# Optimization experiments

Hardware: AMD Instinct MI355X
Metric: run time of the kernel (lower is better)

Reference implementation:

```python
import jax, jax.numpy as jnp
import numpy as np

B, S, D, H = 4, 2048, 512, 8
DH = D // H  # 64


def setup_inputs() -> dict:
    key = jax.random.key(0)
    ks = jax.random.split(key, 7)
    scale = 1.0 / np.sqrt(D)
    return {
        "in_query": jax.random.normal(ks[0], (B, S, D), dtype=jnp.float32),
        "in_key": jax.random.normal(ks[1], (B, S, D), dtype=jnp.float32),
        "in_value": jax.random.normal(ks[2], (B, S, D), dtype=jnp.float32),
        "W_q": jax.random.normal(ks[3], (D, D), dtype=jnp.float32) * scale,
        "W_k": jax.random.normal(ks[4], (D, D), dtype=jnp.float32) * scale,
        "W_v": jax.random.normal(ks[5], (D, D), dtype=jnp.float32) * scale,
        "W_out": jax.random.normal(ks[6], (D, D), dtype=jnp.float32) * scale,
    }


def _split_heads(x):
    # [B, S, D] -> [B, H, S, DH]
    return x.reshape(B, S, H, DH).transpose(0, 2, 1, 3)


def reference(in_query, in_key, in_value, W_q, W_k, W_v, W_out):
    q = _split_heads(in_query @ W_q)   # [B,H,S,DH]
    k = _split_heads(in_key @ W_k)
    v = _split_heads(in_value @ W_v)
    scores = jnp.einsum("bhqd,bhkd->bhqk", q, k) / jnp.sqrt(jnp.float32(DH))
    attn = jax.nn.softmax(scores, axis=-1)  # dropout p=0 -> identity
    out = jnp.einsum("bhqk,bhkd->bhqd", attn, v)  # [B,H,S,DH]
    out = out.transpose(0, 2, 1, 3).reshape(B, S, D)
    return out @ W_out
```

## Files before the change

### kernel.cpp

```cpp
#include <hip/hip_runtime.h>
#include <hip/hip_bf16.h>
#include <cstdint>
#include <cstddef>


typedef __bf16 bf16;
typedef __attribute__((ext_vector_type(8))) __bf16 bf16x8;
typedef __attribute__((ext_vector_type(4))) __bf16 bf16x4;
typedef __attribute__((ext_vector_type(4))) float floatx4;

#define MFMA16(a, b, c) __builtin_amdgcn_mfma_f32_16x16x32_bf16(a, b, c, 0, 0, 0)

#define GLD16(gp, lp)                                              \
  __builtin_amdgcn_global_load_lds(                                \
      (const __attribute__((address_space(1))) unsigned int*)(gp), \
      (__attribute__((address_space(3))) unsigned int*)(lp), 16, 0, 0)

__device__ __forceinline__ void split2(float x, bf16& hi, bf16& lo) {
  hi = (bf16)x;
  lo = (bf16)(x - (float)hi);
}

__global__ __launch_bounds__(256) void k_split_w(
    const float* __restrict__ Wq, const float* __restrict__ Wk,
    const float* __restrict__ Wv, const float* __restrict__ Wo,
    bf16* __restrict__ wt_hi, bf16* __restrict__ wt_lo) {
  __shared__ float tile[64][65];
  const int w = blockIdx.z;
  const float* W = (w == 0) ? Wq : (w == 1) ? Wk : (w == 2) ? Wv : Wo;
  const int kb = blockIdx.y * 64, nb = blockIdx.x * 64;
  const int tid = threadIdx.x;
  const int col = tid & 63, rbase = tid >> 6;
#pragma unroll
  for (int i = 0; i < 16; i++) {
    int row = rbase + i * 4;
    tile[row][col] = W[(size_t)(kb + row) * 512 + nb + col];
  }
  __syncthreads();
#pragma unroll
  for (int i = 0; i < 16; i++) {
    int nrow = rbase + i * 4;
    float v = tile[col][nrow];
    bf16 hi, lo;
    split2(v, hi, lo);
    size_t o = (size_t)w * 262144 + (size_t)(nb + nrow) * 512 + (kb + col);
    wt_hi[o] = hi;
    wt_lo[o] = lo;
  }
}

__global__ __launch_bounds__(256) void k_proj_qkv(
    const float* __restrict__ Xq, const float* __restrict__ Xk,
    const float* __restrict__ Xv,
    const bf16* __restrict__ wt_hi, const bf16* __restrict__ wt_lo,
    bf16* __restrict__ Q_hi, bf16* __restrict__ Q_lo,
    bf16* __restrict__ K_hi, bf16* __restrict__ K_lo,
    bf16* __restrict__ Vt) {
  const int P = blockIdx.x;
  const int c_all = P >> 5, within = P & 31;
  const int n_idx = within >> 3, i8 = within & 7;
  const int which = c_all >> 3;
  const int g = ((c_all & 7) << 3) | i8;
  const int m0 = g * 128, n0 = n_idx * 128;

  const float* X = (which == 0) ? Xq : (which == 1) ? Xk : Xv;
  const uint8_t* Bhb = (const uint8_t*)(wt_hi + (size_t)which * 262144);
  const uint8_t* Blb = (const uint8_t*)(wt_lo + (size_t)which * 262144);
  const uint8_t* Xb = (const uint8_t*)X;
  const int tid = threadIdx.x, wave = tid >> 6, lane = tid & 63;
  const int l15 = lane & 15, l4 = lane >> 4;
  const int Am0 = (wave & 1) * 64, Bn0 = (wave >> 1) * 64;

  __shared__ float sA[128 * 32];
  __shared__ bf16 sBh[128 * 32], sBl[128 * 32];

  int aoff[4], adst[4];
#pragma unroll
  for (int p = 0; p < 4; p++) {
    int slot = p * 256 + tid;
    int row = slot >> 3, phys = slot & 7, lg = phys ^ (row & 7);
    aoff[p] = (m0 + row) * 2048 + lg * 16;
    adst[p] = slot * 16;
  }
  int boff[2], bdst[2];
#pragma unroll
  for (int p = 0; p < 2; p++) {
    int slot = p * 256 + tid;
    int row = slot >> 2, phys = slot & 3, lg = phys ^ (row & 3);
    boff[p] = (n0 + row) * 1024 + lg * 16;
    bdst[p] = slot * 16;
  }

  floatx4 acc[4][4];
#pragma unroll
  for (int i = 0; i < 4; i++)
#pragma unroll
    for (int j = 0; j < 4; j++) acc[i][j] = {0.f, 0.f, 0.f, 0.f};

  for (int kb = 0; kb < 512; kb += 32) {
    __syncthreads();
#pragma unroll
    for (int p = 0; p < 4; p++) GLD16(Xb + aoff[p] + kb * 4, (char*)sA + adst[p]);
#pragma unroll
    for (int p = 0; p < 2; p++) {
      GLD16(Bhb + boff[p] + kb * 2, (char*)sBh + bdst[p]);
      GLD16(Blb + boff[p] + kb * 2, (char*)sBl + bdst[p]);
    }
    __syncthreads();

    bf16x8 ah[4], al[4];
#pragma unroll
    for (int mt = 0; mt < 4; mt++) {
      int row = Am0 + mt * 16 + l15, r7 = row & 7;
      const float* f0 = (const float*)((const char*)sA + row * 128 + (((2 * l4) ^ r7) * 16));
      const float* f1 = (const float*)((const char*)sA + row * 128 + (((2 * l4 + 1) ^ r7) * 16));
#pragma unroll
      for (int j = 0; j < 4; j++) {
        bf16 h, l;
        split2(f0[j], h, l);
        ah[mt][j] = h; al[mt][j] = l;
        split2(f1[j], h, l);
        ah[mt][4 + j] = h; al[mt][4 + j] = l;
      }
    }
#pragma unroll
    for (int nt = 0; nt < 4; nt++) {
      int row = Bn0 + nt * 16 + l15, r3 = row & 3;
      bf16x8 bh = *(const bf16x8*)((const char*)sBh + row * 64 + ((l4 ^ r3) * 16));
      bf16x8 bl = *(const bf16x8*)((const char*)sBl + row * 64 + ((l4 ^ r3) * 16));
#pragma unroll
      for (int mt = 0; mt < 4; mt++) {
        acc[mt][nt] = MFMA16(ah[mt], bh, acc[mt][nt]);
        acc[mt][nt] = MFMA16(ah[mt], bl, acc[mt][nt]);
        acc[mt][nt] = MFMA16(al[mt], bh, acc[mt][nt]);
      }
    }
  }

  const float scale = (which == 0) ? 0.125f : (which == 1) ? 1.44269504f : 1.0f;
#pragma unroll
  for (int mt = 0; mt < 4; mt++) {
#pragma unroll
    for (int nt = 0; nt < 4; nt++) {
      int m_base = m0 + Am0 + mt * 16 + l4 * 4;
      int n = n0 + Bn0 + nt * 16 + l15;
      int h = (n >> 6) & 7, d = n & 63;
      if (which == 2) {
        int b = m_base >> 11, s = m_base & 2047;
        bf16x4 pv;
#pragma unroll
        for (int r = 0; r < 4; r++) pv[r] = (bf16)acc[mt][nt][r];
        *(bf16x4*)&Vt[((size_t)(b * 8 + h) * 64 + d) * 2048 + s] = pv;
      } else {
#pragma unroll
        for (int r = 0; r < 4; r++) {
          int m = m_base + r;
          int b = m >> 11, s = m & 2047;
          float v = acc[mt][nt][r] * scale;
          bf16 hi, lo;
          split2(v, hi, lo);
          size_t o = ((size_t)(b * 8 + h) * 2048 + s) * 64 + d;
          if (which == 0) { Q_hi[o] = hi; Q_lo[o] = lo; }
          else           { K_hi[o] = hi; K_lo[o] = lo; }
        }
      }
    }
  }
}

__global__ __launch_bounds__(256) void k_flash(
    const bf16* __restrict__ Q_hi, const bf16* __restrict__ Q_lo,
    const bf16* __restrict__ K_hi, const bf16* __restrict__ K_lo,
    const bf16* __restrict__ Vt,
    bf16* __restrict__ O_hi, bf16* __restrict__ O_lo) {
  const int P = blockIdx.x;
  const int hi4 = P >> 8, rem = P & 255;
  const int qt = rem >> 3;
  const int bh = hi4 * 8 + (rem & 7);
  const int b = bh >> 3, h = bh & 7;
  const int tid = threadIdx.x, wave = tid >> 6, lane = tid & 63;
  const int l15 = lane & 15, l4 = lane >> 4;
  const int qrow = qt * 64 + wave * 16;

  __shared__ bf16 sKh[64 * 64], sKl[64 * 64];
  __shared__ bf16 sV[64 * 64];
  __shared__ bf16 sP[4][16][72];

  const bf16* qbh = Q_hi + ((size_t)bh * 2048 + qrow + l15) * 64 + l4 * 8;
  const bf16* qbl = Q_lo + ((size_t)bh * 2048 + qrow + l15) * 64 + l4 * 8;
  bf16x8 qh[2], ql[2];
  qh[0] = *(const bf16x8*)qbh;
  qh[1] = *(const bf16x8*)(qbh + 32);
  ql[0] = *(const bf16x8*)qbl;
  ql[1] = *(const bf16x8*)(qbl + 32);

  const uint8_t* Khb = (const uint8_t*)K_hi + (size_t)bh * 2048 * 128;
  const uint8_t* Klb = (const uint8_t*)K_lo + (size_t)bh * 2048 * 128;
  const uint8_t* Vb = (const uint8_t*)Vt + (size_t)bh * 64 * 4096;
  int koff[2], voff[2], dst[2];
#pragma unroll
  for (int p = 0; p < 2; p++) {
    int slot = p * 256 + tid;
    int row = slot >> 3, phys = slot & 7, lg = phys ^ (row & 7);
    koff[p] = row * 128 + lg * 16;
    voff[p] = row * 4096 + lg * 16;
    dst[p] = slot * 16;
  }

  float l_i = 0.f;
  floatx4 oacc[4] = {{0.f, 0.f, 0.f, 0.f}, {0.f, 0.f, 0.f, 0.f},
                     {0.f, 0.f, 0.f, 0.f}, {0.f, 0.f, 0.f, 0.f}};

  for (int j0 = 0; j0 < 2048; j0 += 64) {
    __syncthreads();
#pragma unroll
    for (int p = 0; p < 2; p++) {
      GLD16(Khb + (size_t)j0 * 128 + koff[p], (char*)sKh + dst[p]);
      GLD16(Klb + (size_t)j0 * 128 + koff[p], (char*)sKl + dst[p]);
      GLD16(Vb + j0 * 2 + voff[p], (char*)sV + dst[p]);
    }
    __syncthreads();

    floatx4 sc[4] = {{-24.f, -24.f, -24.f, -24.f}, {-24.f, -24.f, -24.f, -24.f},
                     {-24.f, -24.f, -24.f, -24.f}, {-24.f, -24.f, -24.f, -24.f}};
    const int r7 = l15 & 7;
#pragma unroll
    for (int ks = 0; ks < 2; ks++) {
#pragma unroll
      for (int nt = 0; nt < 4; nt++) {
        int off = (nt * 16 + l15) * 128 + (((ks * 4 + l4) ^ r7) * 16);
        bf16x8 kh = *(const bf16x8*)((const char*)sKh + off);
        bf16x8 kl = *(const bf16x8*)((const char*)sKl + off);
        sc[nt] = MFMA16(kh, qh[ks], sc[nt]);
        sc[nt] = MFMA16(kl, qh[ks], sc[nt]);
        sc[nt] = MFMA16(kh, ql[ks], sc[nt]);
      }
    }

    float ssum = 0.f;
#pragma unroll
    for (int nt = 0; nt < 4; nt++) {
      bf16x4 pk;
#pragma unroll
      for (int r = 0; r < 4; r++) {
        float p = __builtin_amdgcn_exp2f(sc[nt][r]);
        ssum += p;
        pk[r] = (bf16)p;
      }
      *(bf16x4*)&sP[wave][l15][nt * 16 + l4 * 4] = pk;
    }
    l_i += ssum;

#pragma unroll
    for (int ks = 0; ks < 2; ks++) {
      bf16x8 pa = *(const bf16x8*)&sP[wave][l15][ks * 32 + l4 * 8];
#pragma unroll
      for (int nt = 0; nt < 4; nt++) {
        int off = (nt * 16 + l15) * 128 + (((ks * 4 + l4) ^ r7) * 16);
        bf16x8 bv = *(const bf16x8*)((const char*)sV + off);
        oacc[nt] = MFMA16(pa, bv, oacc[nt]);
      }
    }
  }

  l_i += __shfl_xor(l_i, 16, 64);
  l_i += __shfl_xor(l_i, 32, 64);
  float rl[4];
#pragma unroll
  for (int r = 0; r < 4; r++)
    rl[r] = 1.0f / __shfl(l_i, (lane & 48) | (l4 * 4 + r), 64);
#pragma unroll
  for (int nt = 0; nt < 4; nt++) {
#pragma unroll
    for (int r = 0; r < 4; r++) {
      float v = oacc[nt][r] * rl[r];
      int gs = qrow + l4 * 4 + r;
      int gd = h * 64 + nt * 16 + l15;
      size_t o = ((size_t)b * 2048 + gs) * 512 + gd;
      bf16 hi, lo;
      split2(v, hi, lo);
      O_hi[o] = hi;
      O_lo[o] = lo;
    }
  }
}

__global__ __launch_bounds__(256) void k_proj_out(
    const bf16* __restrict__ O_hi, const bf16* __restrict__ O_lo,
    const bf16* __restrict__ wt_hi, const bf16* __restrict__ wt_lo,
    float* __restrict__ out) {
  const int P = blockIdx.x;
  const int c = P >> 5, within = P & 31;
  const int n_idx = within >> 3, i8 = within & 7;
  const int g = (c << 3) | i8;
  const int m0 = g * 128, n0 = n_idx * 128;

  const uint8_t* Ahb = (const uint8_t*)O_hi;
  const uint8_t* Alb = (const uint8_t*)O_lo;
  const uint8_t* Bhb = (const uint8_t*)(wt_hi + (size_t)3 * 262144);
  const uint8_t* Blb = (const uint8_t*)(wt_lo + (size_t)3 * 262144);
  const int tid = threadIdx.x, wave = tid >> 6, lane = tid & 63;
  const int l15 = lane & 15, l4 = lane >> 4;
  const int Am0 = (wave & 1) * 64, Bn0 = (wave >> 1) * 64;

  __shared__ bf16 sAh[128 * 32], sAl[128 * 32];
  __shared__ bf16 sBh[128 * 32], sBl[128 * 32];

  int aoff[2], boff[2], dst[2];
#pragma unroll
  for (int p = 0; p < 2; p++) {
    int slot = p * 256 + tid;
    int row = slot >> 2, phys = slot & 3, lg = phys ^ (row & 3);
    aoff[p] = (m0 + row) * 1024 + lg * 16;
    boff[p] = (n0 + row) * 1024 + lg * 16;
    dst[p] = slot * 16;
  }

  floatx4 acc[4][4];
#pragma unroll
  for (int i = 0; i < 4; i++)
#pragma unroll
    for (int j = 0; j < 4; j++) acc[i][j] = {0.f, 0.f, 0.f, 0.f};

  for (int kb = 0; kb < 512; kb += 32) {
    __syncthreads();
#pragma unroll
    for (int p = 0; p < 2; p++) {
      GLD16(Ahb + aoff[p] + kb * 2, (char*)sAh + dst[p]);
      GLD16(Alb + aoff[p] + kb * 2, (char*)sAl + dst[p]);
      GLD16(Bhb + boff[p] + kb * 2, (char*)sBh + dst[p]);
      GLD16(Blb + boff[p] + kb * 2, (char*)sBl + dst[p]);
    }
    __syncthreads();

    bf16x8 ah[4], al[4];
#pragma unroll
    for (int mt = 0; mt < 4; mt++) {
      int row = Am0 + mt * 16 + l15, r3 = row & 3;
      ah[mt] = *(const bf16x8*)((const char*)sAh + row * 64 + ((l4 ^ r3) * 16));
      al[mt] = *(const bf16x8*)((const char*)sAl + row * 64 + ((l4 ^ r3) * 16));
    }
#pragma unroll
    for (int nt = 0; nt < 4; nt++) {
      int row = Bn0 + nt * 16 + l15, r3 = row & 3;
      bf16x8 bh = *(const bf16x8*)((const char*)sBh + row * 64 + ((l4 ^ r3) * 16));
      bf16x8 bl = *(const bf16x8*)((const char*)sBl + row * 64 + ((l4 ^ r3) * 16));
#pragma unroll
      for (int mt = 0; mt < 4; mt++) {
        acc[mt][nt] = MFMA16(ah[mt], bh, acc[mt][nt]);
        acc[mt][nt] = MFMA16(ah[mt], bl, acc[mt][nt]);
        acc[mt][nt] = MFMA16(al[mt], bh, acc[mt][nt]);
      }
    }
  }
#pragma unroll
  for (int mt = 0; mt < 4; mt++) {
#pragma unroll
    for (int nt = 0; nt < 4; nt++) {
#pragma unroll
      for (int r = 0; r < 4; r++) {
        int m = m0 + Am0 + mt * 16 + l4 * 4 + r;
        int n = n0 + Bn0 + nt * 16 + l15;
        out[(size_t)m * 512 + n] = acc[mt][nt][r];
      }
    }
  }
}

extern "C" void kernel_launch(void* const* d_in, const int* in_sizes, int n_in,
                              void* d_out, int out_size, void* d_ws, size_t ws_size,
                              hipStream_t stream) {
  (void)in_sizes; (void)n_in; (void)out_size; (void)ws_size;
  const float* Xq = (const float*)d_in[0];
  const float* Xk = (const float*)d_in[1];
  const float* Xv = (const float*)d_in[2];
  const float* Wq = (const float*)d_in[3];
  const float* Wk = (const float*)d_in[4];
  const float* Wv = (const float*)d_in[5];
  const float* Wo = (const float*)d_in[6];
  float* out = (float*)d_out;

  char* ws = (char*)d_ws;
  size_t off = 0;
  auto alloc = [&](size_t n) {
    void* p = ws + off;
    off += (n + 255) & ~(size_t)255;
    return p;
  };
  const size_t NW = 4 * 262144;
  const size_t NE = 4194304;
  bf16* wt_hi = (bf16*)alloc(NW * 2);
  bf16* wt_lo = (bf16*)alloc(NW * 2);
  bf16* Qh = (bf16*)alloc(NE * 2);
  bf16* Ql = (bf16*)alloc(NE * 2);
  bf16* Kh = (bf16*)alloc(NE * 2);
  bf16* Kl = (bf16*)alloc(NE * 2);
  bf16* Vt = (bf16*)alloc(NE * 2);
  bf16* Oh = (bf16*)alloc(NE * 2);
  bf16* Ol = (bf16*)alloc(NE * 2);

  k_split_w<<<dim3(8, 8, 4), dim3(256), 0, stream>>>(Wq, Wk, Wv, Wo, wt_hi, wt_lo);
  k_proj_qkv<<<dim3(768), dim3(256), 0, stream>>>(Xq, Xk, Xv, wt_hi, wt_lo,
                                                  Qh, Ql, Kh, Kl, Vt);
  k_flash<<<dim3(1024), dim3(256), 0, stream>>>(Qh, Ql, Kh, Kl, Vt, Oh, Ol);
  k_proj_out<<<dim3(256), dim3(256), 0, stream>>>(Oh, Ol, wt_hi, wt_lo, out);
}
```

Before: 241.5 us.

## Split flash attention over key tiles per wave with in-register P and cross-wave reduction

The flash kernel now has each wave own a 32-key slice of a 128-key tile for all 64 queries, instead of owning 16 queries across a 64-key tile. The score output layout feeds straight into the PV MFMA as the A operand, so the shared-memory round-trip for P is gone. V is written pre-permuted so that key ordering matches the register layout. The cost is four times the oacc registers, a cross-wave reduction of O and row sums at the end, and launch bounds that request two blocks per SM.

```diff
diff --git a/kernel.cpp b/kernel.cpp
--- a/kernel.cpp
+++ b/kernel.cpp
@@ -146,11 +146,13 @@
       int n = n0 + Bn0 + nt * 16 + l15;
       int h = (n >> 6) & 7, d = n & 63;
       if (which == 2) {
-        int b = m_base >> 11, s = m_base & 2047;
+        int kbase = m_base & 2047, b = m_base >> 11;
+        int a32 = kbase & ~31, v = (kbase >> 2) & 7;
+        int sbase = a32 + 8 * (v & 3) + 4 * (v >> 2);
         bf16x4 pv;
 #pragma unroll
         for (int r = 0; r < 4; r++) pv[r] = (bf16)acc[mt][nt][r];
-        *(bf16x4*)&Vt[((size_t)(b * 8 + h) * 64 + d) * 2048 + s] = pv;
+        *(bf16x4*)&Vt[((size_t)(b * 8 + h) * 64 + d) * 2048 + sbase] = pv;
       } else {
 #pragma unroll
         for (int r = 0; r < 4; r++) {
@@ -168,7 +170,7 @@
   }
 }
 
-__global__ __launch_bounds__(256) void k_flash(
+__global__ __launch_bounds__(256, 2) void k_flash(
     const bf16* __restrict__ Q_hi, const bf16* __restrict__ Q_lo,
     const bf16* __restrict__ K_hi, const bf16* __restrict__ K_lo,
     const bf16* __restrict__ Vt,
@@ -180,107 +182,171 @@
   const int b = bh >> 3, h = bh & 7;
   const int tid = threadIdx.x, wave = tid >> 6, lane = tid & 63;
   const int l15 = lane & 15, l4 = lane >> 4;
-  const int qrow = qt * 64 + wave * 16;
-
-  __shared__ bf16 sKh[64 * 64], sKl[64 * 64];
-  __shared__ bf16 sV[64 * 64];
-  __shared__ bf16 sP[4][16][72];
-
-  const bf16* qbh = Q_hi + ((size_t)bh * 2048 + qrow + l15) * 64 + l4 * 8;
-  const bf16* qbl = Q_lo + ((size_t)bh * 2048 + qrow + l15) * 64 + l4 * 8;
-  bf16x8 qh[2], ql[2];
-  qh[0] = *(const bf16x8*)qbh;
-  qh[1] = *(const bf16x8*)(qbh + 32);
-  ql[0] = *(const bf16x8*)qbl;
-  ql[1] = *(const bf16x8*)(qbl + 32);
+  const int q0 = qt * 64;
+
+  __shared__ bf16 sKh[128 * 64];
+  __shared__ bf16 sKl[128 * 64];
+  __shared__ bf16 sV[64 * 128];
+
+  bf16x8 qh[4][2], ql[4][2];
+#pragma unroll
+  for (int nt = 0; nt < 4; nt++) {
+    const bf16* ph = Q_hi + ((size_t)bh * 2048 + q0 + nt * 16 + l15) * 64 + l4 * 8;
+    const bf16* pl = Q_lo + ((size_t)bh * 2048 + q0 + nt * 16 + l15) * 64 + l4 * 8;
+    qh[nt][0] = *(const bf16x8*)ph;
+    qh[nt][1] = *(const bf16x8*)(ph + 32);
+    ql[nt][0] = *(const bf16x8*)pl;
+    ql[nt][1] = *(const bf16x8*)(pl + 32);
+  }
 
   const uint8_t* Khb = (const uint8_t*)K_hi + (size_t)bh * 2048 * 128;
   const uint8_t* Klb = (const uint8_t*)K_lo + (size_t)bh * 2048 * 128;
   const uint8_t* Vb = (const uint8_t*)Vt + (size_t)bh * 64 * 4096;
-  int koff[2], voff[2], dst[2];
-#pragma unroll
-  for (int p = 0; p < 2; p++) {
+  int koff[4], voff[4], dst[4];
+#pragma unroll
+  for (int p = 0; p < 4; p++) {
     int slot = p * 256 + tid;
-    int row = slot >> 3, phys = slot & 7, lg = phys ^ (row & 7);
-    koff[p] = row * 128 + lg * 16;
-    voff[p] = row * 4096 + lg * 16;
+    {
+      int row = slot >> 3, phys = slot & 7, lg = phys ^ (row & 7);
+      koff[p] = row * 128 + lg * 16;
+    }
+    {
+      int row = slot >> 4, phys = slot & 15, lg = phys ^ (row & 15);
+      voff[p] = row * 4096 + lg * 16;
+    }
     dst[p] = slot * 16;
   }
 
-  float l_i = 0.f;
-  floatx4 oacc[4] = {{0.f, 0.f, 0.f, 0.f}, {0.f, 0.f, 0.f, 0.f},
-                     {0.f, 0.f, 0.f, 0.f}, {0.f, 0.f, 0.f, 0.f}};
-
-  for (int j0 = 0; j0 < 2048; j0 += 64) {
-    __syncthreads();
-#pragma unroll
-    for (int p = 0; p < 2; p++) {
+  float lp[4] = {0.f, 0.f, 0.f, 0.f};
+  floatx4 oacc[4][4];
+#pragma unroll
+  for (int i = 0; i < 4; i++)
+#pragma unroll
+    for (int j = 0; j < 4; j++) oacc[i][j] = {0.f, 0.f, 0.f, 0.f};
+
+  for (int j0 = 0; j0 < 2048; j0 += 128) {
+    __syncthreads();
+#pragma unroll
+    for (int p = 0; p < 4; p++) {
       GLD16(Khb + (size_t)j0 * 128 + koff[p], (char*)sKh + dst[p]);
       GLD16(Klb + (size_t)j0 * 128 + koff[p], (char*)sKl + dst[p]);
-      GLD16(Vb + j0 * 2 + voff[p], (char*)sV + dst[p]);
-    }
-    __syncthreads();
-
-    floatx4 sc[4] = {{-24.f, -24.f, -24.f, -24.f}, {-24.f, -24.f, -24.f, -24.f},
-                     {-24.f, -24.f, -24.f, -24.f}, {-24.f, -24.f, -24.f, -24.f}};
-    const int r7 = l15 & 7;
-#pragma unroll
-    for (int ks = 0; ks < 2; ks++) {
-#pragma unroll
-      for (int nt = 0; nt < 4; nt++) {
-        int off = (nt * 16 + l15) * 128 + (((ks * 4 + l4) ^ r7) * 16);
+      GLD16(Vb + (size_t)j0 * 2 + voff[p], (char*)sV + dst[p]);
+    }
+    __syncthreads();
+
+    floatx4 sc[2][4];
+#pragma unroll
+    for (int kt = 0; kt < 2; kt++)
+#pragma unroll
+      for (int nt = 0; nt < 4; nt++) sc[kt][nt] = {0.f, 0.f, 0.f, 0.f};
+#pragma unroll
+    for (int kt = 0; kt < 2; kt++) {
+      int row = wave * 32 + kt * 16 + l15;
+      int r7 = row & 7;
+#pragma unroll
+      for (int ks = 0; ks < 2; ks++) {
+        int off = row * 128 + (((ks * 4 + l4) ^ r7) * 16);
         bf16x8 kh = *(const bf16x8*)((const char*)sKh + off);
         bf16x8 kl = *(const bf16x8*)((const char*)sKl + off);
-        sc[nt] = MFMA16(kh, qh[ks], sc[nt]);
-        sc[nt] = MFMA16(kl, qh[ks], sc[nt]);
-        sc[nt] = MFMA16(kh, ql[ks], sc[nt]);
-      }
-    }
-
-    float ssum = 0.f;
-#pragma unroll
-    for (int nt = 0; nt < 4; nt++) {
-      bf16x4 pk;
+#pragma unroll
+        for (int nt = 0; nt < 4; nt++) {
+          sc[kt][nt] = MFMA16(kh, qh[nt][ks], sc[kt][nt]);
+          sc[kt][nt] = MFMA16(kl, qh[nt][ks], sc[kt][nt]);
+          sc[kt][nt] = MFMA16(kh, ql[nt][ks], sc[kt][nt]);
+        }
+      }
+    }
+
+    bf16x8 pf[4];
+#pragma unroll
+    for (int nt = 0; nt < 4; nt++) {
 #pragma unroll
       for (int r = 0; r < 4; r++) {
-        float p = __builtin_amdgcn_exp2f(sc[nt][r]);
-        ssum += p;
-        pk[r] = (bf16)p;
-      }
-      *(bf16x4*)&sP[wave][l15][nt * 16 + l4 * 4] = pk;
-    }
-    l_i += ssum;
-
-#pragma unroll
-    for (int ks = 0; ks < 2; ks++) {
-      bf16x8 pa = *(const bf16x8*)&sP[wave][l15][ks * 32 + l4 * 8];
+        float p0 = __builtin_amdgcn_exp2f(sc[0][nt][r]);
+        float p1 = __builtin_amdgcn_exp2f(sc[1][nt][r]);
+        lp[nt] += p0 + p1;
+        pf[nt][r] = (bf16)p0;
+        pf[nt][4 + r] = (bf16)p1;
+      }
+    }
+
+#pragma unroll
+    for (int nt = 0; nt < 4; nt++) {
+      int row = nt * 16 + l15;
+      int off = row * 256 + (((wave * 4 + l4) ^ l15) * 16);
+      bf16x8 bv = *(const bf16x8*)((const char*)sV + off);
+#pragma unroll
+      for (int mq = 0; mq < 4; mq++)
+        oacc[mq][nt] = MFMA16(pf[mq], bv, oacc[mq][nt]);
+    }
+  }
+
+#pragma unroll
+  for (int nt = 0; nt < 4; nt++) {
+    lp[nt] += __shfl_xor(lp[nt], 16, 64);
+    lp[nt] += __shfl_xor(lp[nt], 32, 64);
+  }
+  float* lbuf = (float*)sV;
+  floatx4* red0 = (floatx4*)sKh;
+  floatx4* red1 = (floatx4*)sKl;
+  __syncthreads();
+  if (l4 == 0) {
+#pragma unroll
+    for (int nt = 0; nt < 4; nt++) lbuf[wave * 64 + nt * 16 + l15] = lp[nt];
+  }
+  if (wave == 2) {
+#pragma unroll
+    for (int i = 0; i < 16; i++) red0[i * 64 + lane] = oacc[i >> 2][i & 3];
+  }
+  if (wave == 3) {
+#pragma unroll
+    for (int i = 0; i < 16; i++) red1[i * 64 + lane] = oacc[i >> 2][i & 3];
+  }
+  __syncthreads();
+  if (wave == 0) {
+#pragma unroll
+    for (int i = 0; i < 16; i++) oacc[i >> 2][i & 3] += red0[i * 64 + lane];
+  }
+  if (wave == 1) {
+#pragma unroll
+    for (int i = 0; i < 16; i++) oacc[i >> 2][i & 3] += red1[i * 64 + lane];
+  }
+  __syncthreads();
+  if (wave == 1) {
+#pragma unroll
+    for (int i = 0; i < 16; i++) red0[i * 64 + lane] = oacc[i >> 2][i & 3];
+  }
+  __syncthreads();
+  if (wave == 0) {
+#pragma unroll
+    for (int i = 0; i < 16; i++) oacc[i >> 2][i & 3] += red0[i * 64 + lane];
+    float lt[4];
+#pragma unroll
+    for (int nt = 0; nt < 4; nt++)
+      lt[nt] = lbuf[nt * 16 + l15] + lbuf[64 + nt * 16 + l15] +
+               lbuf[128 + nt * 16 + l15] + lbuf[192 + nt * 16 + l15];
+    float rl[4][4];
+#pragma unroll
+    for (int mq = 0; mq < 4; mq++)
+#pragma unroll
+      for (int r = 0; r < 4; r++)
+        rl[mq][r] = 1.0f / __shfl(lt[mq], (lane & 48) | (l4 * 4 + r), 64);
+#pragma unroll
+    for (int mq = 0; mq < 4; mq++) {
 #pragma unroll
       for (int nt = 0; nt < 4; nt++) {
-        int off = (nt * 16 + l15) * 128 + (((ks * 4 + l4) ^ r7) * 16);
-        bf16x8 bv = *(const bf16x8*)((const char*)sV + off);
-        oacc[nt] = MFMA16(pa, bv, oacc[nt]);
-      }
-    }
-  }
-
-  l_i += __shfl_xor(l_i, 16, 64);
-  l_i += __shfl_xor(l_i, 32, 64);
-  float rl[4];
-#pragma unroll
-  for (int r = 0; r < 4; r++)
-    rl[r] = 1.0f / __shfl(l_i, (lane & 48) | (l4 * 4 + r), 64);
-#pragma unroll
-  for (int nt = 0; nt < 4; nt++) {
-#pragma unroll
-    for (int r = 0; r < 4; r++) {
-      float v = oacc[nt][r] * rl[r];
-      int gs = qrow + l4 * 4 + r;
-      int gd = h * 64 + nt * 16 + l15;
-      size_t o = ((size_t)b * 2048 + gs) * 512 + gd;
-      bf16 hi, lo;
-      split2(v, hi, lo);
-      O_hi[o] = hi;
-      O_lo[o] = lo;
+#pragma unroll
+        for (int r = 0; r < 4; r++) {
+          float v = oacc[mq][nt][r] * rl[mq][r];
+          int gs = q0 + mq * 16 + l4 * 4 + r;
+          int gd = h * 64 + nt * 16 + l15;
+          size_t o = ((size_t)b * 2048 + gs) * 512 + gd;
+          bf16 hi, lo;
+          split2(v, hi, lo);
+          O_hi[o] = hi;
+          O_lo[o] = lo;
+        }
+      }
     }
   }
 }
```

New measurement: 233.1 us. -3.5%, faster.
